# Kernel optimization log

Hardware: AMD Instinct MI355X
Metric: run time of the kernel (lower is better)

## Reference

```python
import jax, jax.numpy as jnp
import numpy as np

C = 256
K = 8
D = C // K  # qk projection dim = 32


def setup_inputs() -> dict:
    key = jax.random.key(0)
    ks = jax.random.split(key, 9)
    s = 1.0 / np.sqrt(C)
    x = jax.random.normal(ks[0], (4, C, 64, 64), dtype=jnp.float32)
    Wq = jax.random.normal(ks[1], (D, C), dtype=jnp.float32) * s
    bq = jnp.zeros((D,), dtype=jnp.float32)
    Wk = jax.random.normal(ks[2], (D, C), dtype=jnp.float32) * s
    bk = jnp.zeros((D,), dtype=jnp.float32)
    Wv = jax.random.normal(ks[3], (C, C), dtype=jnp.float32) * s
    bv = jnp.zeros((C,), dtype=jnp.float32)
    Wp = jax.random.normal(ks[4], (C, C), dtype=jnp.float32) * s
    bp = jnp.zeros((C,), dtype=jnp.float32)
    gamma = jnp.float32(0.5)  # nonzero so output depends on attention path
    return {"x": x, "Wq": Wq, "bq": bq, "Wk": Wk, "bk": bk,
            "Wv": Wv, "bv": bv, "Wp": Wp, "bp": bp, "gamma": gamma}


def reference(x, Wq, bq, Wk, bk, Wv, bv, Wp, bp, gamma):
    B, Cc, H, W = x.shape
    N = H * W
    xf = x.reshape(B, Cc, N)  # (B, C, N); 1x1 conv == per-pixel linear
    q = jnp.einsum('dc,bcn->bnd', Wq, xf) + bq  # (B, N, D)
    k = jnp.einsum('dc,bcn->bdn', Wk, xf) + bk[None, :, None]  # (B, D, N)
    v = jnp.einsum('dc,bcn->bdn', Wv, xf) + bv[None, :, None]  # (B, C, N)
    scale = 1.0 / jnp.sqrt(jnp.float32(q.shape[-1]))
    attn = jax.nn.softmax(jnp.einsum('bnd,bdm->bnm', q, k) * scale, axis=-1)  # (B, Nq, Nk)
    out = jnp.einsum('bcm,bnm->bcn', v, attn)  # (B, C, Nq)
    out = jnp.einsum('oc,bcn->bon', Wp, out) + bp[None, :, None]
    out = out.reshape(B, Cc, H, W)
    return x + gamma * out
```

## Files before the change

kernel.cpp:

```cpp
#include <hip/hip_runtime.h>
#include <math.h>

#define BB 4
#define CC 256
#define DD 32
#define NN 4096

typedef __attribute__((ext_vector_type(8))) short short8;
typedef __attribute__((ext_vector_type(4))) float floatx4;
typedef __attribute__((ext_vector_type(16))) float floatx16;
typedef __attribute__((ext_vector_type(4))) int intx4;
typedef __attribute__((ext_vector_type(2))) int intx2;

#define SCALEF (0.17677669529663687f * 1.4426950408889634f)

__device__ __forceinline__ ushort f2bf(float f) {
    unsigned int u = __builtin_bit_cast(unsigned int, f);
    u += 0x7FFFu + ((u >> 16) & 1u);
    return (ushort)(u >> 16);
}
__device__ __forceinline__ int pk_trunc(float a, float b) {
    return (int)__builtin_amdgcn_perm(__builtin_bit_cast(unsigned, b),
                                      __builtin_bit_cast(unsigned, a),
                                      0x07060302u);
}
__device__ __forceinline__ float fast_exp2(float x) {
#if __has_builtin(__builtin_amdgcn_exp2f)
    return __builtin_amdgcn_exp2f(x);
#else
    return exp2f(x);
#endif
}
__device__ __forceinline__ void plswap(int& a, int& b) {
#if __has_builtin(__builtin_amdgcn_permlane32_swap)
    intx2 r = __builtin_amdgcn_permlane32_swap(a, b, false, false);
    a = r[0]; b = r[1];
#else
    const int lane = threadIdx.x & 63;
    const bool hi = lane >= 32;
    int a2 = __shfl(a, lane ^ 32);
    int b2 = __shfl(b, lane ^ 32);
    int na = hi ? b2 : a;
    int nb = hi ? b : a2;
    a = na; b = nb;
#endif
}

#define QTP 264
__global__ __launch_bounds__(640) void qkv_fused(
    const float* __restrict__ x,
    const float* __restrict__ Wq, const float* __restrict__ bq,
    const float* __restrict__ Wk, const float* __restrict__ bk,
    const float* __restrict__ Wv, const float* __restrict__ bv,
    const float* __restrict__ Wp, ushort* __restrict__ Wpb,
    ushort* __restrict__ qb, ushort* __restrict__ kb, ushort* __restrict__ vb)
{
    __shared__ ushort tile[64 * QTP];

    const int t = threadIdx.x;
    const int wave = t >> 6;
    const int lane = t & 63;
    const int l15 = lane & 15, qd = lane >> 4;
    const int b = blockIdx.y;
    const int n0 = blockIdx.x * 64;
    const int mt = wave;

    const int bid = blockIdx.y * gridDim.x + blockIdx.x;
    if (bid < 64 && t < 256) {
        const int e = (bid * 256 + t) * 4;
        const int row = e >> 8, col = e & 255;
        const floatx4 w = *(const floatx4*)(Wp + (size_t)row * CC + col);
        int2 d;
        d.x = pk_trunc(w[0], w[1]);
        d.y = pk_trunc(w[2], w[3]);
        *(int2*)(Wpb + (size_t)(col >> 3) * (CC * 8) + row * 8 + (col & 7)) = d;
    }

    if (t < 512) {
        const int tt = t & 255;
        const int cl = (tt >> 4) * 4;
        const int nl = (tt & 15) * 4;
        const int pb = (t >> 8) * 2;
        #pragma unroll
        for (int pp = 0; pp < 2; ++pp) {
            const int cp = (pb + pp) * 64;
            const float* src = x + ((size_t)b * CC + cp + cl) * NN + n0 + nl;
            floatx4 v[4];
            #pragma unroll
            for (int i = 0; i < 4; ++i) v[i] = *(const floatx4*)(src + (size_t)i * NN);
            #pragma unroll
            for (int j = 0; j < 4; ++j) {
                *(int*)&tile[(nl + j) * QTP + cp + cl]     = pk_trunc(v[0][j], v[1][j]);
                *(int*)&tile[(nl + j) * QTP + cp + cl + 2] = pk_trunc(v[2][j], v[3][j]);
            }
        }
    }
    __syncthreads();

    const float* wr[2];
    if (mt == 0) {
        wr[0] = Wq + (size_t)l15 * CC;
        wr[1] = Wq + (size_t)(16 + l15) * CC;
    } else if (mt == 1) {
        wr[0] = Wk + (size_t)l15 * CC;
        wr[1] = Wk + (size_t)(16 + l15) * CC;
    } else {
        wr[0] = Wv + (size_t)((mt - 2) * 32 + l15) * CC;
        wr[1] = Wv + (size_t)((mt - 2) * 32 + 16 + l15) * CC;
    }

    floatx4 z = {0.f, 0.f, 0.f, 0.f};
    floatx4 acc[2][4];
    #pragma unroll
    for (int fm = 0; fm < 2; ++fm)
        #pragma unroll
        for (int fn = 0; fn < 4; ++fn) acc[fm][fn] = z;

    #pragma unroll
    for (int k0 = 0; k0 < CC; k0 += 32) {
        short8 af[2], bfr[4];
        #pragma unroll
        for (int f = 0; f < 2; ++f) {
            const float* p = wr[f] + k0 + qd * 8;
            float w[8];
            #pragma unroll
            for (int j = 0; j < 8; ++j) w[j] = p[j];
            if (mt == 0) {
                #pragma unroll
                for (int j = 0; j < 8; ++j) w[j] *= SCALEF;
            }
            intx4 d;
            d[0] = pk_trunc(w[0], w[1]); d[1] = pk_trunc(w[2], w[3]);
            d[2] = pk_trunc(w[4], w[5]); d[3] = pk_trunc(w[6], w[7]);
            af[f] = __builtin_bit_cast(short8, d);
        }
        #pragma unroll
        for (int fn = 0; fn < 4; ++fn)
            bfr[fn] = *(const short8*)&tile[(fn * 16 + l15) * QTP + k0 + qd * 8];
        #pragma unroll
        for (int fm = 0; fm < 2; ++fm)
            #pragma unroll
            for (int fn = 0; fn < 4; ++fn)
                acc[fm][fn] = __builtin_amdgcn_mfma_f32_16x16x32_bf16(af[fm], bfr[fn], acc[fm][fn], 0, 0, 0);
    }

    #pragma unroll
    for (int fm = 0; fm < 2; ++fm) {
        const int o0 = fm * 16 + qd * 4;
        if (mt == 0) {
            const floatx4 bb = *(const floatx4*)(bq + o0);
            #pragma unroll
            for (int fn = 0; fn < 4; ++fn) {
                ushort4 h;
                h.x = f2bf(acc[fm][fn][0] + bb[0] * SCALEF);
                h.y = f2bf(acc[fm][fn][1] + bb[1] * SCALEF);
                h.z = f2bf(acc[fm][fn][2] + bb[2] * SCALEF);
                h.w = f2bf(acc[fm][fn][3] + bb[3] * SCALEF);
                *(ushort4*)(qb + ((size_t)b * NN + n0 + fn * 16 + l15) * DD + o0) = h;
            }
        } else if (mt == 1) {
            const floatx4 bb = *(const floatx4*)(bk + o0);
            #pragma unroll
            for (int fn = 0; fn < 4; ++fn) {
                ushort4 h;
                h.x = f2bf(acc[fm][fn][0] + bb[0]);
                h.y = f2bf(acc[fm][fn][1] + bb[1]);
                h.z = f2bf(acc[fm][fn][2] + bb[2]);
                h.w = f2bf(acc[fm][fn][3] + bb[3]);
                *(ushort4*)(kb + (size_t)b * NN * DD
                                 + (size_t)(n0 / 16 + fn) * 512
                                 + (fm * 2 + (qd >> 1)) * 128
                                 + l15 * 8 + (qd & 1) * 4) = h;
            }
        } else {
            const int oc0 = (mt - 2) * 32 + o0;
            const floatx4 bb = *(const floatx4*)(bv + oc0);
            #pragma unroll
            for (int r = 0; r < 4; ++r)
                #pragma unroll
                for (int fn = 0; fn < 4; ++fn)
                    vb[(size_t)b * CC * NN
                       + (size_t)(n0 / 16 + fn) * (CC * 16)
                       + (oc0 + r) * 16 + l15] = f2bf(acc[fm][fn][r] + bb[r]);
        }
    }
}

__global__ __launch_bounds__(256, 2) void attn_mfma(
    const ushort* __restrict__ qb, const ushort* __restrict__ kb,
    const ushort* __restrict__ vb, ushort* __restrict__ aoT)
{
    __shared__ float red[2][8192];
    __shared__ float lred[2][64];

    const int t = threadIdx.x;
    const int kh = t >> 6;
    const int lane = t & 63;
    const int l31 = lane & 31;
    const bool hi = lane >= 32;
    const int hib = hi ? 8 : 0;
    const int slot = blockIdx.x;
    const int b = slot >> 1;
    const int qt = (slot & 1) * 32 + blockIdx.y;
    const int q0 = qt * 64;
    const int c0 = blockIdx.z * 128;

    short8 qf[2][2];
    #pragma unroll
    for (int qg = 0; qg < 2; ++qg)
        #pragma unroll
        for (int dh = 0; dh < 2; ++dh)
            qf[qg][dh] = *(const short8*)(qb + ((size_t)b * NN + q0 + qg * 32 + l31) * DD + dh * 16 + hib);

    const ushort* krow = kb + (size_t)b * NN * DD + (size_t)kh * 64 * 512
                            + (l31 >> 4) * 512 + (l31 & 15) * 8 + hib * 16;
    const ushort* vrow = vb + (size_t)b * CC * NN + (size_t)kh * 64 * (CC * 16)
                            + (c0 + l31) * 16 + hib;

    floatx16 z16 = {0.f,0.f,0.f,0.f,0.f,0.f,0.f,0.f,0.f,0.f,0.f,0.f,0.f,0.f,0.f,0.f};
    floatx16 acc[2][4];
    #pragma unroll
    for (int qg = 0; qg < 2; ++qg)
        #pragma unroll
        for (int cg = 0; cg < 4; ++cg) acc[qg][cg] = z16;
    float lsum[2] = {0.f, 0.f};

    for (int kt = 0; kt < 32; ++kt) {
        short8 kf0 = *(const short8*)(krow);
        short8 kf1 = *(const short8*)(krow + 256);
        krow += 1024;
        short8 vf[4][2];
        #pragma unroll
        for (int cg = 0; cg < 4; ++cg)
            #pragma unroll
            for (int k2 = 0; k2 < 2; ++k2)
                vf[cg][k2] = *(const short8*)(vrow + cg * 512 + k2 * (CC * 16));
        vrow += 2 * (CC * 16);

        short8 ptB[2][2];
        #pragma unroll
        for (int qg = 0; qg < 2; ++qg) {
            floatx16 s = __builtin_amdgcn_mfma_f32_32x32x16_bf16(kf0, qf[qg][0], z16, 0, 0, 0);
            s = __builtin_amdgcn_mfma_f32_32x32x16_bf16(kf1, qf[qg][1], s, 0, 0, 0);

            float e[16];
            #pragma unroll
            for (int r = 0; r < 16; ++r) e[r] = fast_exp2(s[r]);

            lsum[qg] += (((e[0]+e[1])+(e[2]+e[3]))+((e[4]+e[5])+(e[6]+e[7])))
                      + (((e[8]+e[9])+(e[10]+e[11]))+((e[12]+e[13])+(e[14]+e[15])));

            int a0 = pk_trunc(e[0], e[1]),  b0 = pk_trunc(e[2], e[3]);
            int c0w = pk_trunc(e[4], e[5]), d0 = pk_trunc(e[6], e[7]);
            plswap(a0, c0w);
            plswap(b0, d0);
            intx4 f0 = {a0, b0, c0w, d0};
            ptB[qg][0] = __builtin_bit_cast(short8, f0);

            int a1 = pk_trunc(e[8], e[9]),   b1 = pk_trunc(e[10], e[11]);
            int c1 = pk_trunc(e[12], e[13]), d1 = pk_trunc(e[14], e[15]);
            plswap(a1, c1);
            plswap(b1, d1);
            intx4 f1 = {a1, b1, c1, d1};
            ptB[qg][1] = __builtin_bit_cast(short8, f1);
        }

        __builtin_amdgcn_s_setprio(1);
        #pragma unroll
        for (int cg = 0; cg < 4; ++cg)
            #pragma unroll
            for (int qg = 0; qg < 2; ++qg) {
                acc[qg][cg] = __builtin_amdgcn_mfma_f32_32x32x16_bf16(vf[cg][0], ptB[qg][0], acc[qg][cg], 0, 0, 0);
                acc[qg][cg] = __builtin_amdgcn_mfma_f32_32x32x16_bf16(vf[cg][1], ptB[qg][1], acc[qg][cg], 0, 0, 0);
            }
        __builtin_amdgcn_s_setprio(0);
    }

    #pragma unroll
    for (int qg = 0; qg < 2; ++qg)
        lsum[qg] += __shfl(lsum[qg], lane ^ 32);

    if (kh & 1) {
        const int s = kh >> 1;
        #pragma unroll
        for (int qg = 0; qg < 2; ++qg)
            #pragma unroll
            for (int cg = 0; cg < 4; ++cg)
                #pragma unroll
                for (int r = 0; r < 16; ++r)
                    red[s][((qg * 4 + cg) * 16 + r) * 64 + lane] = acc[qg][cg][r];
        if (!hi)
            #pragma unroll
            for (int qg = 0; qg < 2; ++qg) lred[s][qg * 32 + l31] = lsum[qg];
    }
    __syncthreads();
    if (!(kh & 1)) {
        const int s = kh >> 1;
        #pragma unroll
        for (int qg = 0; qg < 2; ++qg) {
            #pragma unroll
            for (int cg = 0; cg < 4; ++cg)
                #pragma unroll
                for (int r = 0; r < 16; ++r)
                    acc[qg][cg][r] += red[s][((qg * 4 + cg) * 16 + r) * 64 + lane];
            lsum[qg] += lred[s][qg * 32 + l31];
        }
    }
    __syncthreads();
    if (kh == 2) {
        #pragma unroll
        for (int qg = 0; qg < 2; ++qg)
            #pragma unroll
            for (int cg = 0; cg < 4; ++cg)
                #pragma unroll
                for (int r = 0; r < 16; ++r)
                    red[0][((qg * 4 + cg) * 16 + r) * 64 + lane] = acc[qg][cg][r];
        if (!hi)
            #pragma unroll
            for (int qg = 0; qg < 2; ++qg) lred[0][qg * 32 + l31] = lsum[qg];
    }
    __syncthreads();
    if (kh == 0) {
        #pragma unroll
        for (int qg = 0; qg < 2; ++qg) {
            #pragma unroll
            for (int cg = 0; cg < 4; ++cg)
                #pragma unroll
                for (int r = 0; r < 16; ++r)
                    acc[qg][cg][r] += red[0][((qg * 4 + cg) * 16 + r) * 64 + lane];
            lsum[qg] += lred[0][qg * 32 + l31];
        }
        #pragma unroll
        for (int qg = 0; qg < 2; ++qg) {
            const float inv = 1.0f / lsum[qg];
            const int n = q0 + qg * 32 + l31;
            ushort* dstb = aoT + (size_t)b * NN * CC;
            #pragma unroll
            for (int cg = 0; cg < 4; ++cg) {
                #pragma unroll
                for (int rq = 0; rq < 4; ++rq) {
                    ushort4 h;
                    h.x = f2bf(acc[qg][cg][rq * 4 + 0] * inv);
                    h.y = f2bf(acc[qg][cg][rq * 4 + 1] * inv);
                    h.z = f2bf(acc[qg][cg][rq * 4 + 2] * inv);
                    h.w = f2bf(acc[qg][cg][rq * 4 + 3] * inv);
                    *(ushort4*)(dstb + (size_t)(c0 / 8 + cg * 4 + rq) * (NN * 8)
                                     + (size_t)n * 8 + (hi ? 4 : 0)) = h;
                }
            }
        }
    }
}

__global__ __launch_bounds__(256) void proj_mfma(
    const ushort* __restrict__ aoT, const ushort* __restrict__ Wpb,
    const float* __restrict__ bp, const float* __restrict__ x,
    const float* __restrict__ gamma, float* __restrict__ out)
{
    const int t = threadIdx.x;
    const int wave = t >> 6;
    const int lane = t & 63;
    const int l15 = lane & 15;
    const int qd = lane >> 4;
    const int b = blockIdx.z;
    const int m0 = blockIdx.y * 32;
    const int n0 = blockIdx.x * 128 + wave * 32;

    floatx4 z = {0.f, 0.f, 0.f, 0.f};
    floatx4 acc[2][2];
    acc[0][0] = z; acc[0][1] = z; acc[1][0] = z; acc[1][1] = z;

    const ushort* ab = aoT + (size_t)b * NN * CC;

    #pragma unroll
    for (int k0 = 0; k0 < CC; k0 += 32) {
        const size_t cblk = (size_t)(k0 / 8 + qd);
        short8 af[2], bfr[2];
        af[0]  = *(const short8*)(Wpb + cblk * (CC * 8) + (m0 + l15) * 8);
        af[1]  = *(const short8*)(Wpb + cblk * (CC * 8) + (m0 + 16 + l15) * 8);
        bfr[0] = *(const short8*)(ab + cblk * (NN * 8) + (size_t)(n0 + l15) * 8);
        bfr[1] = *(const short8*)(ab + cblk * (NN * 8) + (size_t)(n0 + 16 + l15) * 8);
        #pragma unroll
        for (int fm = 0; fm < 2; ++fm)
            #pragma unroll
            for (int fn = 0; fn < 2; ++fn)
                acc[fm][fn] = __builtin_amdgcn_mfma_f32_16x16x32_bf16(af[fm], bfr[fn], acc[fm][fn], 0, 0, 0);
    }

    const float g = gamma[0];
    #pragma unroll
    for (int fm = 0; fm < 2; ++fm) {
        #pragma unroll
        for (int r = 0; r < 4; ++r) {
            int m = m0 + fm * 16 + qd * 4 + r;
            float bpv = bp[m];
            #pragma unroll
            for (int fn = 0; fn < 2; ++fn) {
                size_t addr = ((size_t)b * CC + m) * NN + n0 + fn * 16 + l15;
                out[addr] = fmaf(g, acc[fm][fn][r] + bpv, x[addr]);
            }
        }
    }
}

extern "C" void kernel_launch(void* const* d_in, const int* in_sizes, int n_in,
                              void* d_out, int out_size, void* d_ws, size_t ws_size,
                              hipStream_t stream)
{
    const float* x     = (const float*)d_in[0];
    const float* Wq    = (const float*)d_in[1];
    const float* bq    = (const float*)d_in[2];
    const float* Wk    = (const float*)d_in[3];
    const float* bk    = (const float*)d_in[4];
    const float* Wv    = (const float*)d_in[5];
    const float* bv    = (const float*)d_in[6];
    const float* Wp    = (const float*)d_in[7];
    const float* bp    = (const float*)d_in[8];
    const float* gamma = (const float*)d_in[9];
    float* out = (float*)d_out;

    ushort* qbw = (ushort*)d_ws;
    ushort* kbw = qbw + (size_t)BB * NN * DD;
    ushort* vbw = kbw + (size_t)BB * NN * DD;
    ushort* aoT = vbw + (size_t)BB * CC * NN;
    ushort* Wpb = aoT + (size_t)BB * NN * CC;

    qkv_fused<<<dim3(NN / 64, BB), 640, 0, stream>>>(x, Wq, bq, Wk, bk, Wv, bv, Wp, Wpb, qbw, kbw, vbw);
    attn_mfma<<<dim3(8, 32, 2), 256, 0, stream>>>(qbw, kbw, vbw, aoT);
    proj_mfma<<<dim3(NN / 128, CC / 32, BB), 256, 0, stream>>>(aoT, Wpb, bp, x, gamma, out);
}
```

Before: 152.9 us.

## Fuse output projection into attention kernel via shared-memory attention tile

Merges the attention and projection kernels. Each 512-thread block now covers both 128-channel halves for its 64 queries, writes the normalized bf16 attention output into shared memory (reusing the reduction buffer), and then runs the Wp projection plus residual directly. This removes the global round trip of the attention output and one kernel launch. In exchange the grid shrinks from 512 to 256 blocks, each with twice the threads and twice the shared memory, which may lower occupancy and parallelism.

```diff
diff --git a/kernel.cpp b/kernel.cpp
--- a/kernel.cpp
+++ b/kernel.cpp
@@ -186,15 +186,20 @@
     }
 }
 
-__global__ __launch_bounds__(256, 2) void attn_mfma(
+__global__ __launch_bounds__(512, 2) void attn_proj(
     const ushort* __restrict__ qb, const ushort* __restrict__ kb,
-    const ushort* __restrict__ vb, ushort* __restrict__ aoT)
+    const ushort* __restrict__ vb, const ushort* __restrict__ Wpb,
+    const float* __restrict__ bp, const float* __restrict__ x,
+    const float* __restrict__ gamma, float* __restrict__ out)
 {
-    __shared__ float red[2][8192];
-    __shared__ float lred[2][64];
+    __shared__ float red[2][2][8192];
+    __shared__ float lred[2][2][64];
+    ushort* ao_u = (ushort*)&red[0][0][0];
 
     const int t = threadIdx.x;
-    const int kh = t >> 6;
+    const int w = t >> 6;
+    const int kh = w & 3;
+    const int ch = w >> 2;
     const int lane = t & 63;
     const int l31 = lane & 31;
     const bool hi = lane >= 32;
@@ -203,7 +208,7 @@
     const int b = slot >> 1;
     const int qt = (slot & 1) * 32 + blockIdx.y;
     const int q0 = qt * 64;
-    const int c0 = blockIdx.z * 128;
+    const int c0 = ch * 128;
 
     short8 qf[2][2];
     #pragma unroll
@@ -288,10 +293,10 @@
             for (int cg = 0; cg < 4; ++cg)
                 #pragma unroll
                 for (int r = 0; r < 16; ++r)
-                    red[s][((qg * 4 + cg) * 16 + r) * 64 + lane] = acc[qg][cg][r];
+                    red[ch][s][((qg * 4 + cg) * 16 + r) * 64 + lane] = acc[qg][cg][r];
         if (!hi)
             #pragma unroll
-            for (int qg = 0; qg < 2; ++qg) lred[s][qg * 32 + l31] = lsum[qg];
+            for (int qg = 0; qg < 2; ++qg) lred[ch][s][qg * 32 + l31] = lsum[qg];
     }
     __syncthreads();
     if (!(kh & 1)) {
@@ -302,8 +307,8 @@
             for (int cg = 0; cg < 4; ++cg)
                 #pragma unroll
                 for (int r = 0; r < 16; ++r)
-                    acc[qg][cg][r] += red[s][((qg * 4 + cg) * 16 + r) * 64 + lane];
-            lsum[qg] += lred[s][qg * 32 + l31];
+                    acc[qg][cg][r] += red[ch][s][((qg * 4 + cg) * 16 + r) * 64 + lane];
+            lsum[qg] += lred[ch][s][qg * 32 + l31];
         }
     }
     __syncthreads();
@@ -314,10 +319,10 @@
             for (int cg = 0; cg < 4; ++cg)
                 #pragma unroll
                 for (int r = 0; r < 16; ++r)
-                    red[0][((qg * 4 + cg) * 16 + r) * 64 + lane] = acc[qg][cg][r];
+                    red[ch][0][((qg * 4 + cg) * 16 + r) * 64 + lane] = acc[qg][cg][r];
         if (!hi)
             #pragma unroll
-            for (int qg = 0; qg < 2; ++qg) lred[0][qg * 32 + l31] = lsum[qg];
+            for (int qg = 0; qg < 2; ++qg) lred[ch][0][qg * 32 + l31] = lsum[qg];
     }
     __syncthreads();
     if (kh == 0) {
@@ -327,14 +332,17 @@
             for (int cg = 0; cg < 4; ++cg)
                 #pragma unroll
                 for (int r = 0; r < 16; ++r)
-                    acc[qg][cg][r] += red[0][((qg * 4 + cg) * 16 + r) * 64 + lane];
-            lsum[qg] += lred[0][qg * 32 + l31];
-        }
+                    acc[qg][cg][r] += red[ch][0][((qg * 4 + cg) * 16 + r) * 64 + lane];
+            lsum[qg] += lred[ch][0][qg * 32 + l31];
+        }
+    }
+    __syncthreads();
+
+    if (kh == 0) {
         #pragma unroll
         for (int qg = 0; qg < 2; ++qg) {
             const float inv = 1.0f / lsum[qg];
-            const int n = q0 + qg * 32 + l31;
-            ushort* dstb = aoT + (size_t)b * NN * CC;
+            const int nl = qg * 32 + l31;
             #pragma unroll
             for (int cg = 0; cg < 4; ++cg) {
                 #pragma unroll
@@ -344,62 +352,33 @@
                     h.y = f2bf(acc[qg][cg][rq * 4 + 1] * inv);
                     h.z = f2bf(acc[qg][cg][rq * 4 + 2] * inv);
                     h.w = f2bf(acc[qg][cg][rq * 4 + 3] * inv);
-                    *(ushort4*)(dstb + (size_t)(c0 / 8 + cg * 4 + rq) * (NN * 8)
-                                     + (size_t)n * 8 + (hi ? 4 : 0)) = h;
+                    *(ushort4*)&ao_u[(((ch * 16 + cg * 4 + rq) * 64) + nl) * 8 + (hi ? 4 : 0)] = h;
                 }
             }
         }
     }
-}
-
-__global__ __launch_bounds__(256) void proj_mfma(
-    const ushort* __restrict__ aoT, const ushort* __restrict__ Wpb,
-    const float* __restrict__ bp, const float* __restrict__ x,
-    const float* __restrict__ gamma, float* __restrict__ out)
-{
-    const int t = threadIdx.x;
-    const int wave = t >> 6;
-    const int lane = t & 63;
-    const int l15 = lane & 15;
-    const int qd = lane >> 4;
-    const int b = blockIdx.z;
-    const int m0 = blockIdx.y * 32;
-    const int n0 = blockIdx.x * 128 + wave * 32;
-
-    floatx4 z = {0.f, 0.f, 0.f, 0.f};
-    floatx4 acc[2][2];
-    acc[0][0] = z; acc[0][1] = z; acc[1][0] = z; acc[1][1] = z;
-
-    const ushort* ab = aoT + (size_t)b * NN * CC;
-
-    #pragma unroll
-    for (int k0 = 0; k0 < CC; k0 += 32) {
-        const size_t cblk = (size_t)(k0 / 8 + qd);
-        short8 af[2], bfr[2];
-        af[0]  = *(const short8*)(Wpb + cblk * (CC * 8) + (m0 + l15) * 8);
-        af[1]  = *(const short8*)(Wpb + cblk * (CC * 8) + (m0 + 16 + l15) * 8);
-        bfr[0] = *(const short8*)(ab + cblk * (NN * 8) + (size_t)(n0 + l15) * 8);
-        bfr[1] = *(const short8*)(ab + cblk * (NN * 8) + (size_t)(n0 + 16 + l15) * 8);
-        #pragma unroll
-        for (int fm = 0; fm < 2; ++fm)
-            #pragma unroll
-            for (int fn = 0; fn < 2; ++fn)
-                acc[fm][fn] = __builtin_amdgcn_mfma_f32_16x16x32_bf16(af[fm], bfr[fn], acc[fm][fn], 0, 0, 0);
-    }
-
+    __syncthreads();
+
+    const int m0w = w * 32;
+    floatx16 pacc0 = z16, pacc1 = z16;
+    #pragma unroll
+    for (int kc = 0; kc < 16; ++kc) {
+        const int cb = kc * 2 + (hi ? 1 : 0);
+        short8 af  = *(const short8*)(Wpb + (size_t)cb * (CC * 8) + (m0w + l31) * 8);
+        short8 bf0 = *(const short8*)&ao_u[(cb * 64 + l31) * 8];
+        short8 bf1 = *(const short8*)&ao_u[(cb * 64 + 32 + l31) * 8];
+        pacc0 = __builtin_amdgcn_mfma_f32_32x32x16_bf16(af, bf0, pacc0, 0, 0, 0);
+        pacc1 = __builtin_amdgcn_mfma_f32_32x32x16_bf16(af, bf1, pacc1, 0, 0, 0);
+    }
     const float g = gamma[0];
     #pragma unroll
-    for (int fm = 0; fm < 2; ++fm) {
-        #pragma unroll
-        for (int r = 0; r < 4; ++r) {
-            int m = m0 + fm * 16 + qd * 4 + r;
-            float bpv = bp[m];
-            #pragma unroll
-            for (int fn = 0; fn < 2; ++fn) {
-                size_t addr = ((size_t)b * CC + m) * NN + n0 + fn * 16 + l15;
-                out[addr] = fmaf(g, acc[fm][fn][r] + bpv, x[addr]);
-            }
-        }
+    for (int r = 0; r < 16; ++r) {
+        const int m = m0w + (r & 3) + 8 * (r >> 2) + (hi ? 4 : 0);
+        const float bpv = bp[m];
+        const size_t a0 = ((size_t)b * CC + m) * NN + q0 + l31;
+        out[a0] = fmaf(g, pacc0[r] + bpv, x[a0]);
+        const size_t a1 = a0 + 32;
+        out[a1] = fmaf(g, pacc1[r] + bpv, x[a1]);
     }
 }
 
@@ -422,10 +401,8 @@
     ushort* qbw = (ushort*)d_ws;
     ushort* kbw = qbw + (size_t)BB * NN * DD;
     ushort* vbw = kbw + (size_t)BB * NN * DD;
-    ushort* aoT = vbw + (size_t)BB * CC * NN;
-    ushort* Wpb = aoT + (size_t)BB * NN * CC;
+    ushort* Wpb = vbw + (size_t)BB * CC * NN;
 
     qkv_fused<<<dim3(NN / 64, BB), 640, 0, stream>>>(x, Wq, bq, Wk, bk, Wv, bv, Wp, Wpb, qbw, kbw, vbw);
-    attn_mfma<<<dim3(8, 32, 2), 256, 0, stream>>>(qbw, kbw, vbw, aoT);
-    proj_mfma<<<dim3(NN / 128, CC / 32, BB), 256, 0, stream>>>(aoT, Wpb, bp, x, gamma, out);
-}
+    attn_proj<<<dim3(8, 32), 512, 0, stream>>>(qbw, kbw, vbw, Wpb, bp, x, gamma, out);
+}
```

After: 150.3 us. No clear change (-1.7%).
